# Performance work log

Hardware: AMD Instinct MI355X
Metric: run time of the kernel (lower is better)

## Reference

```python
import jax, jax.numpy as jnp
import numpy as np

N_NODES = 100000
N_EDGES = 400000
D_IN = 128
D_OUT = 128
BN_EPS = 1e-5


def setup_inputs() -> dict:
    key = jax.random.key(0)
    k1, k2, k3, k4, k5 = jax.random.split(key, 5)
    n_feat = jax.random.normal(k1, (N_NODES, D_IN), dtype=jnp.float32)
    edge_index = jax.random.randint(k2, (2, N_EDGES), 0, N_NODES, dtype=jnp.int32)
    edge_weight = jnp.ones((N_EDGES,), dtype=jnp.float32)
    # learned params: BatchNorm1d affine + Linear(in, out, bias=False)
    gamma = jnp.ones((D_IN,), dtype=jnp.float32) + 0.1 * jax.random.normal(k3, (D_IN,), dtype=jnp.float32)
    beta = 0.1 * jax.random.normal(k4, (D_IN,), dtype=jnp.float32)
    W = jax.random.normal(k5, (D_OUT, D_IN), dtype=jnp.float32) * (1.0 / np.sqrt(D_IN))
    return {"n_feat": n_feat, "edge_index": edge_index, "edge_weight": edge_weight,
            "gamma": gamma, "beta": beta, "W": W}


def reference(n_feat, edge_index, edge_weight, gamma, beta, W):
    # BatchNorm1d (training-mode batch stats, biased variance) -> ReLU -> Linear (no bias)
    mu = jnp.mean(n_feat, axis=0)
    var = jnp.mean(jnp.square(n_feat - mu), axis=0)
    xh = (n_feat - mu) * jax.lax.rsqrt(var + BN_EPS)
    y = jax.nn.relu(gamma * xh + beta)
    h = y @ W.T  # [N, D_OUT]
    # sparse adjacency matmul: out[row] += w * h[col]
    row, col = edge_index[0], edge_index[1]
    msgs = h[col] * edge_weight[:, None]          # gather, [E, D_OUT]
    agg = jax.ops.segment_sum(msgs, row, num_segments=N_NODES)
    return h * h + agg
```

## Files before the change

### kernel.cpp

```cpp
#include <hip/hip_runtime.h>

#define N_NODES 100000
#define N_EDGES 400000
#define D 128
#define BN_EPS 1e-5f
#define ELL_CAP 32

#define NSTAT 64
#define CS_BLOCKS 625
#define CS_ITER 20

#define WS_STATS   0
#define WS_HB      (NSTAT * 256)
#define WS_DEG2    (WS_HB + N_NODES * D / 2)
#define WS_ELL2    (WS_DEG2 + N_NODES)
#define WS_ELL2_END (WS_ELL2 + N_NODES * ELL_CAP * 2)
#define WS_WB      WS_ELL2_END
#define WS_SCL     (WS_WB + 8192)
#define WS_SHF     (WS_SCL + 128)
#define WS_ELL_END2 (WS_SHF + 128)
#define WS_SCALE   (NSTAT * 256)
#define WS_SHIFT   (WS_SCALE + 128)
#define WS_WT      (WS_SHIFT + 128)
#define WS_H       (WS_WT + D * D)
#define WS_DEG     (WS_H + N_NODES * D)
#define WS_ROWPTR  (WS_DEG + N_NODES)
#define WS_CURSOR  (WS_ROWPTR + N_NODES + 1)
#define WS_CSRCOL  (WS_CURSOR + N_NODES)
#define WS_CSRW    (WS_CSRCOL + N_EDGES)
#define WS_END     (WS_CSRW + N_EDGES)

typedef __attribute__((ext_vector_type(8))) short short8;
typedef __attribute__((ext_vector_type(4))) float f32x4;

static __device__ __forceinline__ unsigned short f2bf(float f) {
    union { float f; unsigned u; } v; v.f = f;
    unsigned r = v.u + 0x7FFF + ((v.u >> 16) & 1);
    return (unsigned short)(r >> 16);
}
static __device__ __forceinline__ float bf2f(unsigned short b) {
    union { unsigned u; float f; } v; v.u = ((unsigned)b) << 16;
    return v.f;
}
static __device__ __forceinline__ unsigned short f2h(float f) {
    union { _Float16 h; unsigned short u; } v; v.h = (_Float16)f;
    return v.u;
}
static __device__ __forceinline__ float h2f(unsigned short u) {
    union { unsigned short u; _Float16 h; } v; v.u = u;
    return (float)v.h;
}

__global__ __launch_bounds__(256) void colstats_kernel(const float* __restrict__ x,
                                                       float* __restrict__ stats,
                                                       int* __restrict__ deg) {
    int tid = blockIdx.x * 256 + threadIdx.x;
    if (deg && tid < N_NODES) deg[tid] = 0;
    const int NTH = CS_BLOCKS * 256;
    const float4* x4 = (const float4*)x;
    float4 v[CS_ITER];
    #pragma unroll
    for (int i = 0; i < CS_ITER; i++) v[i] = x4[tid + i * NTH];
    float4 s = {0.f, 0.f, 0.f, 0.f};
    float4 q = {0.f, 0.f, 0.f, 0.f};
    #pragma unroll
    for (int i = 0; i < CS_ITER; i++) {
        s.x += v[i].x; s.y += v[i].y; s.z += v[i].z; s.w += v[i].w;
        q.x += v[i].x * v[i].x; q.y += v[i].y * v[i].y;
        q.z += v[i].z * v[i].z; q.w += v[i].w * v[i].w;
    }

    __shared__ float4 ss[256];
    __shared__ float4 sq[256];
    ss[threadIdx.x] = s;
    sq[threadIdx.x] = q;
    __syncthreads();
    if (threadIdx.x < 32) {
        float4 a = ss[threadIdx.x];
        float4 b = sq[threadIdx.x];
        for (int i = 32; i < 256; i += 32) {
            float4 t1 = ss[threadIdx.x + i];
            float4 t2 = sq[threadIdx.x + i];
            a.x += t1.x; a.y += t1.y; a.z += t1.z; a.w += t1.w;
            b.x += t2.x; b.y += t2.y; b.z += t2.z; b.w += t2.w;
        }
        float* st = stats + (blockIdx.x % NSTAT) * 256;
        int colb = (threadIdx.x * 4) & 127;
        atomicAdd(&st[colb + 0], a.x);
        atomicAdd(&st[colb + 1], a.y);
        atomicAdd(&st[colb + 2], a.z);
        atomicAdd(&st[colb + 3], a.w);
        atomicAdd(&st[128 + colb + 0], b.x);
        atomicAdd(&st[128 + colb + 1], b.y);
        atomicAdd(&st[128 + colb + 2], b.z);
        atomicAdd(&st[128 + colb + 3], b.w);
    }
}

__global__ __launch_bounds__(256) void fill_ell2_kernel(const int* __restrict__ ei,
                                                        const float* __restrict__ ew,
                                                        int* __restrict__ deg,
                                                        int2* __restrict__ ell2) {
    int e = blockIdx.x * 256 + threadIdx.x;
    if (e >= N_EDGES) return;
    int r = ei[e];
    int c = ei[N_EDGES + e];
    float w = ew[e];
    int slot = atomicAdd(&deg[r], 1);
    if (slot < ELL_CAP) ell2[r * ELL_CAP + slot] = make_int2(c, __float_as_int(w));
}

__global__ __launch_bounds__(256) void convw_finalize_kernel(const float* __restrict__ W,
                                                             const float* __restrict__ stats,
                                                             const float* __restrict__ gamma,
                                                             const float* __restrict__ beta,
                                                             unsigned short* __restrict__ Wb,
                                                             float* __restrict__ scale,
                                                             float* __restrict__ shift) {
    int b = blockIdx.x;
    int t = threadIdx.x;
    if (b < 16) {
        int i = b * 256 + t;
        float4 v = *(const float4*)(W + i * 4);
        ushort4 o;
        o.x = f2bf(v.x); o.y = f2bf(v.y); o.z = f2bf(v.z); o.w = f2bf(v.w);
        *(ushort4*)(Wb + i * 4) = o;
    } else if (t < 128) {
        float sum = 0.f, sq = 0.f;
        #pragma unroll 16
        for (int c = 0; c < NSTAT; c++) {
            sum += stats[c * 256 + t];
            sq  += stats[c * 256 + 128 + t];
        }
        float mu  = sum * (1.0f / N_NODES);
        float var = sq * (1.0f / N_NODES) - mu * mu;
        float sc  = gamma[t] * rsqrtf(var + BN_EPS);
        scale[t] = sc;
        shift[t] = beta[t] - mu * sc;
    }
}

#define YPAD 136
__global__ __launch_bounds__(256, 2) void gemm_mfma4_kernel(const float* __restrict__ x,
                                                            const float* __restrict__ scale,
                                                            const float* __restrict__ shift,
                                                            const unsigned short* __restrict__ Wb,
                                                            unsigned short* __restrict__ hh) {
    __shared__ __align__(16) unsigned short Yl[64 * YPAD];
    int t = threadIdx.x;
    int row0 = blockIdx.x * 64;
    int lane = t & 63;
    int wave = t >> 6;
    int m16  = lane & 15;
    int quad = lane >> 4;
    int wrow0 = wave * 16;
    int c4 = (t & 31) * 4;

    float4 sc = *(const float4*)(scale + c4);
    float4 sh = *(const float4*)(shift + c4);
    float4 xv[8];
    #pragma unroll
    for (int p = 0; p < 8; p++) {
        int r = (t + p * 256) >> 5;
        int grow = row0 + r;
        int srow = grow < N_NODES ? grow : N_NODES - 1;
        xv[p] = *(const float4*)(x + (size_t)srow * D + c4);
    }
    const unsigned short* wb = Wb + m16 * D + quad * 8;
    short8 bfr[4][8];
    #pragma unroll
    for (int kc = 0; kc < 4; kc++) {
        #pragma unroll
        for (int nt = 0; nt < 8; nt++) {
            bfr[kc][nt] = *(const short8*)(wb + nt * 16 * D + kc * 32);
        }
    }
    #pragma unroll
    for (int p = 0; p < 8; p++) {
        int r = (t + p * 256) >> 5;
        ushort4 y;
        y.x = f2bf(fmaxf(fmaf(xv[p].x, sc.x, sh.x), 0.f));
        y.y = f2bf(fmaxf(fmaf(xv[p].y, sc.y, sh.y), 0.f));
        y.z = f2bf(fmaxf(fmaf(xv[p].z, sc.z, sh.z), 0.f));
        y.w = f2bf(fmaxf(fmaf(xv[p].w, sc.w, sh.w), 0.f));
        *(ushort4*)(Yl + r * YPAD + c4) = y;
    }
    __syncthreads();

    f32x4 acc[8];
    #pragma unroll
    for (int nt = 0; nt < 8; nt++) acc[nt] = (f32x4){0.f, 0.f, 0.f, 0.f};

    const unsigned short* yl = Yl + (wrow0 + m16) * YPAD + quad * 8;
    #pragma unroll
    for (int kc = 0; kc < 4; kc++) {
        short8 a = *(const short8*)(yl + kc * 32);
        #pragma unroll
        for (int nt = 0; nt < 8; nt++) {
            acc[nt] = __builtin_amdgcn_mfma_f32_16x16x32_bf16(a, bfr[kc][nt], acc[nt], 0, 0, 0);
        }
    }

    #pragma unroll
    for (int r = 0; r < 4; r++) {
        int grow = row0 + wrow0 + quad * 4 + r;
        if (grow < N_NODES) {
            unsigned short* hrow = hh + (size_t)grow * D + m16;
            #pragma unroll
            for (int nt = 0; nt < 8; nt++) {
                hrow[nt * 16] = f2h(acc[nt][r]);
            }
        }
    }
}

__global__ __launch_bounds__(256) void gather_ell3_kernel(const int* __restrict__ deg,
                                                          const int2* __restrict__ ell2,
                                                          const unsigned short* __restrict__ hh,
                                                          float* __restrict__ out) {
    int lane = threadIdx.x & 15;
    int n = blockIdx.x * 16 + (threadIdx.x >> 4);
    if (n >= N_NODES) return;
    short8 hself = *(const short8*)(hh + (size_t)n * D + lane * 8);
    int dg = deg[n];
    if (dg > ELL_CAP) dg = ELL_CAP;
    int dg16 = dg < 16 ? dg : 16;

    int2 my = make_int2(0, 0);
    if (lane < dg16) my = ell2[n * ELL_CAP + lane];

    float acc[8] = {0.f, 0.f, 0.f, 0.f, 0.f, 0.f, 0.f, 0.f};
    int s = 0;
    for (; s + 4 <= dg16; s += 4) {
        int   c0 = __shfl(my.x, s + 0, 16); float w0 = __int_as_float(__shfl(my.y, s + 0, 16));
        int   c1 = __shfl(my.x, s + 1, 16); float w1 = __int_as_float(__shfl(my.y, s + 1, 16));
        int   c2 = __shfl(my.x, s + 2, 16); float w2 = __int_as_float(__shfl(my.y, s + 2, 16));
        int   c3 = __shfl(my.x, s + 3, 16); float w3 = __int_as_float(__shfl(my.y, s + 3, 16));
        short8 v0 = *(const short8*)(hh + (size_t)c0 * D + lane * 8);
        short8 v1 = *(const short8*)(hh + (size_t)c1 * D + lane * 8);
        short8 v2 = *(const short8*)(hh + (size_t)c2 * D + lane * 8);
        short8 v3 = *(const short8*)(hh + (size_t)c3 * D + lane * 8);
        #pragma unroll
        for (int j = 0; j < 8; j++) {
            acc[j] = fmaf(w0, h2f((unsigned short)v0[j]), acc[j]);
            acc[j] = fmaf(w1, h2f((unsigned short)v1[j]), acc[j]);
            acc[j] = fmaf(w2, h2f((unsigned short)v2[j]), acc[j]);
            acc[j] = fmaf(w3, h2f((unsigned short)v3[j]), acc[j]);
        }
    }
    for (; s < dg16; s++) {
        int c = __shfl(my.x, s, 16);
        float w = __int_as_float(__shfl(my.y, s, 16));
        short8 v = *(const short8*)(hh + (size_t)c * D + lane * 8);
        #pragma unroll
        for (int j = 0; j < 8; j++) acc[j] = fmaf(w, h2f((unsigned short)v[j]), acc[j]);
    }
    for (s = 16; s < dg; s++) {
        int2 cw = ell2[n * ELL_CAP + s];
        float w = __int_as_float(cw.y);
        short8 v = *(const short8*)(hh + (size_t)cw.x * D + lane * 8);
        #pragma unroll
        for (int j = 0; j < 8; j++) acc[j] = fmaf(w, h2f((unsigned short)v[j]), acc[j]);
    }

    float4 a, b;
    {
        float h0 = h2f((unsigned short)hself[0]); float h1 = h2f((unsigned short)hself[1]);
        float h2 = h2f((unsigned short)hself[2]); float h3 = h2f((unsigned short)hself[3]);
        float h4 = h2f((unsigned short)hself[4]); float h5 = h2f((unsigned short)hself[5]);
        float h6 = h2f((unsigned short)hself[6]); float h7 = h2f((unsigned short)hself[7]);
        a.x = fmaf(h0, h0, acc[0]); a.y = fmaf(h1, h1, acc[1]);
        a.z = fmaf(h2, h2, acc[2]); a.w = fmaf(h3, h3, acc[3]);
        b.x = fmaf(h4, h4, acc[4]); b.y = fmaf(h5, h5, acc[5]);
        b.z = fmaf(h6, h6, acc[6]); b.w = fmaf(h7, h7, acc[7]);
    }
    float* o = out + (size_t)n * D + lane * 8;
    *(float4*)o = a;
    *(float4*)(o + 4) = b;
}

__global__ __launch_bounds__(128) void finalize_kernel(const float* __restrict__ stats,
                                                       const float* __restrict__ gamma,
                                                       const float* __restrict__ beta,
                                                       float* __restrict__ scale,
                                                       float* __restrict__ shift) {
    int d = threadIdx.x;
    float sum = 0.f, sq = 0.f;
    #pragma unroll 16
    for (int c = 0; c < NSTAT; c++) {
        sum += stats[c * 256 + d];
        sq  += stats[c * 256 + 128 + d];
    }
    float mu  = sum * (1.0f / N_NODES);
    float var = sq * (1.0f / N_NODES) - mu * mu;
    float sc  = gamma[d] * rsqrtf(var + BN_EPS);
    scale[d] = sc;
    shift[d] = beta[d] - mu * sc;
}

__global__ __launch_bounds__(256) void transposeW_kernel(const float* __restrict__ W,
                                                         float* __restrict__ Wt) {
    int i = blockIdx.x * blockDim.x + threadIdx.x;
    if (i < D * D) {
        int j = i >> 7;
        int k = i & 127;
        Wt[k * D + j] = W[i];
    }
}

template <int WRITE_SQ>
__global__ __launch_bounds__(256) void gemm_kernel(const float* __restrict__ x,
                                                   const float* __restrict__ scale,
                                                   const float* __restrict__ shift,
                                                   const float* __restrict__ Wt,
                                                   float* __restrict__ h,
                                                   float* __restrict__ out) {
    __shared__ float Ws[D * D];
    __shared__ float Ys[32 * D];
    int t = threadIdx.x;
    const float4* Wt4 = (const float4*)Wt;
    float4* Ws4 = (float4*)Ws;
    #pragma unroll 4
    for (int i = t; i < D * D / 4; i += 256) Ws4[i] = Wt4[i];
    int row0 = blockIdx.x * 32;
    const float4* x4 = (const float4*)(x + (size_t)row0 * D);
    float4* Ys4 = (float4*)Ys;
    #pragma unroll 2
    for (int i = t; i < 32 * D / 4; i += 256) {
        int c4 = (i & 31) * 4;
        float4 v = x4[i];
        v.x = fmaxf(fmaf(v.x, scale[c4 + 0], shift[c4 + 0]), 0.f);
        v.y = fmaxf(fmaf(v.y, scale[c4 + 1], shift[c4 + 1]), 0.f);
        v.z = fmaxf(fmaf(v.z, scale[c4 + 2], shift[c4 + 2]), 0.f);
        v.w = fmaxf(fmaf(v.w, scale[c4 + 3], shift[c4 + 3]), 0.f);
        Ys4[i] = v;
    }
    __syncthreads();
    int cg = t & 31;
    int rg = t >> 5;
    float4 acc[4] = {{0,0,0,0},{0,0,0,0},{0,0,0,0},{0,0,0,0}};
    #pragma unroll 2
    for (int k = 0; k < D; k += 4) {
        float4 w0 = *(const float4*)&Ws[(k + 0) * D + cg * 4];
        float4 w1 = *(const float4*)&Ws[(k + 1) * D + cg * 4];
        float4 w2 = *(const float4*)&Ws[(k + 2) * D + cg * 4];
        float4 w3 = *(const float4*)&Ws[(k + 3) * D + cg * 4];
        #pragma unroll
        for (int r = 0; r < 4; r++) {
            float4 y = *(const float4*)&Ys[(rg * 4 + r) * D + k];
            acc[r].x = fmaf(y.x, w0.x, fmaf(y.y, w1.x, fmaf(y.z, w2.x, fmaf(y.w, w3.x, acc[r].x))));
            acc[r].y = fmaf(y.x, w0.y, fmaf(y.y, w1.y, fmaf(y.z, w2.y, fmaf(y.w, w3.y, acc[r].y))));
            acc[r].z = fmaf(y.x, w0.z, fmaf(y.y, w1.z, fmaf(y.z, w2.z, fmaf(y.w, w3.z, acc[r].z))));
            acc[r].w = fmaf(y.x, w0.w, fmaf(y.y, w1.w, fmaf(y.z, w2.w, fmaf(y.w, w3.w, acc[r].w))));
        }
    }
    #pragma unroll
    for (int r = 0; r < 4; r++) {
        size_t row = (size_t)row0 + rg * 4 + r;
        float4 v = acc[r];
        *(float4*)&h[row * D + cg * 4] = v;
        if (WRITE_SQ) {
            float4 sqv = {v.x * v.x, v.y * v.y, v.z * v.z, v.w * v.w};
            *(float4*)&out[row * D + cg * 4] = sqv;
        }
    }
}

__global__ __launch_bounds__(256) void hist_kernel(const int* __restrict__ ei,
                                                   int* __restrict__ deg) {
    int e = blockIdx.x * 256 + threadIdx.x;
    if (e < N_EDGES) atomicAdd(&deg[ei[e]], 1);
}

__global__ __launch_bounds__(1024) void scan_kernel(const int* __restrict__ deg,
                                                    int* __restrict__ row_ptr,
                                                    int* __restrict__ cursor) {
    __shared__ int part[1024];
    int t = threadIdx.x;
    const int CHUNK = 100;
    int base = t * CHUNK;
    int s = 0;
    if (base < N_NODES) {
        for (int i = 0; i < CHUNK; i++) s += deg[base + i];
    }
    part[t] = s;
    __syncthreads();
    for (int off = 1; off < 1024; off <<= 1) {
        int v = (t >= off) ? part[t - off] : 0;
        __syncthreads();
        part[t] += v;
        __syncthreads();
    }
    int pre = (t == 0) ? 0 : part[t - 1];
    if (base < N_NODES) {
        for (int i = 0; i < CHUNK; i++) {
            row_ptr[base + i] = pre;
            cursor[base + i] = pre;
            pre += deg[base + i];
        }
    }
    if (t == 1023) row_ptr[N_NODES] = part[1023];
}

__global__ __launch_bounds__(256) void fill_kernel(const int* __restrict__ ei,
                                                   const float* __restrict__ ew,
                                                   int* __restrict__ cursor,
                                                   int* __restrict__ csr_col,
                                                   float* __restrict__ csr_w) {
    int e = blockIdx.x * 256 + threadIdx.x;
    if (e >= N_EDGES) return;
    int r = ei[e];
    int c = ei[N_EDGES + e];
    int slot = atomicAdd(&cursor[r], 1);
    csr_col[slot] = c;
    csr_w[slot] = ew[e];
}

__global__ __launch_bounds__(256) void gather_kernel(const int* __restrict__ row_ptr,
                                                     const int* __restrict__ csr_col,
                                                     const float* __restrict__ csr_w,
                                                     const float* __restrict__ h,
                                                     float* __restrict__ out) {
    int lane = threadIdx.x & 31;
    int n = blockIdx.x * 8 + (threadIdx.x >> 5);
    if (n >= N_NODES) return;
    int s0 = row_ptr[n];
    int s1 = row_ptr[n + 1];
    float4 acc = {0.f, 0.f, 0.f, 0.f};
    for (int s = s0; s < s1; s++) {
        int c = csr_col[s];
        float w = csr_w[s];
        float4 v = *(const float4*)&h[(size_t)c * D + lane * 4];
        acc.x = fmaf(w, v.x, acc.x);
        acc.y = fmaf(w, v.y, acc.y);
        acc.z = fmaf(w, v.z, acc.z);
        acc.w = fmaf(w, v.w, acc.w);
    }
    float4 hv = *(const float4*)&h[(size_t)n * D + lane * 4];
    float4 o;
    o.x = fmaf(hv.x, hv.x, acc.x);
    o.y = fmaf(hv.y, hv.y, acc.y);
    o.z = fmaf(hv.z, hv.z, acc.z);
    o.w = fmaf(hv.w, hv.w, acc.w);
    *(float4*)&out[(size_t)n * D + lane * 4] = o;
}

__global__ __launch_bounds__(256) void scatter_kernel(const int* __restrict__ ei,
                                                      const float* __restrict__ ew,
                                                      const float* __restrict__ h,
                                                      float* __restrict__ out) {
    int lane = threadIdx.x & 31;
    int e = blockIdx.x * 8 + (threadIdx.x >> 5);
    if (e >= N_EDGES) return;
    int r = ei[e];
    int c = ei[N_EDGES + e];
    float w = ew[e];
    float4 v = *(const float4*)&h[(size_t)c * D + lane * 4];
    float* o = out + (size_t)r * D + lane * 4;
    atomicAdd(o + 0, v.x * w);
    atomicAdd(o + 1, v.y * w);
    atomicAdd(o + 2, v.z * w);
    atomicAdd(o + 3, v.w * w);
}

extern "C" void kernel_launch(void* const* d_in, const int* in_sizes, int n_in,
                              void* d_out, int out_size, void* d_ws, size_t ws_size,
                              hipStream_t stream) {
    const float* n_feat = (const float*)d_in[0];
    const int*   ei     = (const int*)d_in[1];
    const float* ew     = (const float*)d_in[2];
    const float* gamma  = (const float*)d_in[3];
    const float* beta   = (const float*)d_in[4];
    const float* W      = (const float*)d_in[5];
    float* out = (float*)d_out;

    float* ws    = (float*)d_ws;
    float* stats = ws + WS_STATS;

    bool ell_ok = ws_size >= (size_t)WS_ELL_END2 * sizeof(float);
    bool csr_ok = ws_size >= (size_t)WS_END * sizeof(float);

    hipMemsetAsync(stats, 0, NSTAT * 256 * sizeof(float), stream);

    if (ell_ok) {
        unsigned short* hh  = (unsigned short*)(ws + WS_HB);
        int*  deg  = (int*)ws + WS_DEG2;
        int2* ell2 = (int2*)((int*)ws + WS_ELL2);
        unsigned short* Wb = (unsigned short*)(ws + WS_WB);
        float* scl = ws + WS_SCL;
        float* shf = ws + WS_SHF;

        colstats_kernel<<<CS_BLOCKS, 256, 0, stream>>>(n_feat, stats, deg);
        fill_ell2_kernel<<<(N_EDGES + 255) / 256, 256, 0, stream>>>(ei, ew, deg, ell2);
        convw_finalize_kernel<<<17, 256, 0, stream>>>(W, stats, gamma, beta, Wb, scl, shf);
        gemm_mfma4_kernel<<<(N_NODES + 63) / 64, 256, 0, stream>>>(n_feat, scl, shf, Wb, hh);
        gather_ell3_kernel<<<(N_NODES + 15) / 16, 256, 0, stream>>>(deg, ell2, hh, out);
    } else if (csr_ok) {
        float* scale = ws + WS_SCALE;
        float* shift = ws + WS_SHIFT;
        float* Wt    = ws + WS_WT;
        float* h     = ws + WS_H;
        int*   deg     = (int*)ws + WS_DEG;
        int*   row_ptr = (int*)ws + WS_ROWPTR;
        int*   cursor  = (int*)ws + WS_CURSOR;
        int*   csr_col = (int*)ws + WS_CSRCOL;
        float* csr_w   = ws + WS_CSRW;

        colstats_kernel<<<CS_BLOCKS, 256, 0, stream>>>(n_feat, stats, nullptr);
        finalize_kernel<<<1, 128, 0, stream>>>(stats, gamma, beta, scale, shift);
        transposeW_kernel<<<64, 256, 0, stream>>>(W, Wt);
        hipMemsetAsync(deg, 0, N_NODES * sizeof(int), stream);
        gemm_kernel<0><<<N_NODES / 32, 256, 0, stream>>>(n_feat, scale, shift, Wt, h, out);
        hist_kernel<<<(N_EDGES + 255) / 256, 256, 0, stream>>>(ei, deg);
        scan_kernel<<<1, 1024, 0, stream>>>(deg, row_ptr, cursor);
        fill_kernel<<<(N_EDGES + 255) / 256, 256, 0, stream>>>(ei, ew, cursor, csr_col, csr_w);
        gather_kernel<<<(N_NODES + 7) / 8, 256, 0, stream>>>(row_ptr, csr_col, csr_w, h, out);
    } else {
        float* scale = ws + WS_SCALE;
        float* shift = ws + WS_SHIFT;
        float* Wt    = ws + WS_WT;
        float* h     = ws + WS_H;
        colstats_kernel<<<CS_BLOCKS, 256, 0, stream>>>(n_feat, stats, nullptr);
        finalize_kernel<<<1, 128, 0, stream>>>(stats, gamma, beta, scale, shift);
        transposeW_kernel<<<64, 256, 0, stream>>>(W, Wt);
        gemm_kernel<1><<<N_NODES / 32, 256, 0, stream>>>(n_feat, scale, shift, Wt, h, out);
        scatter_kernel<<<(N_EDGES + 7) / 8, 256, 0, stream>>>(ei, ew, h, out);
    }
}
```

Before: 195.1 us.

## Fuse ELL fill with weight conversion, raise GEMM occupancy, batch gather per lane group

Merges the edge-to-ELL fill kernel with the weight-conversion/BN-finalize kernel into one launch, removing a launch gap. The GEMM kernel no longer preloads all B fragments into registers and instead loads them inside the MFMA loop, with launch bounds raised to 4 blocks per SM for higher occupancy. The gather kernel now has each 16-lane group process 4 nodes in an interleaved loop, so more independent loads are in flight. This trades register-held weights for repeated global/L1 loads and adds per-node divergence checks in the gather. It also reads ELL entries beyond each node's degree, which are likely uninitialized but only shuffled when used.

```diff
diff --git a/kernel.cpp b/kernel.cpp
--- a/kernel.cpp
+++ b/kernel.cpp
@@ -9,6 +9,7 @@
 #define NSTAT 64
 #define CS_BLOCKS 625
 #define CS_ITER 20
+#define FILL_BLOCKS 1563
 
 #define WS_STATS   0
 #define WS_HB      (NSTAT * 256)
@@ -97,30 +98,29 @@
     }
 }
 
-__global__ __launch_bounds__(256) void fill_ell2_kernel(const int* __restrict__ ei,
-                                                        const float* __restrict__ ew,
-                                                        int* __restrict__ deg,
-                                                        int2* __restrict__ ell2) {
-    int e = blockIdx.x * 256 + threadIdx.x;
-    if (e >= N_EDGES) return;
-    int r = ei[e];
-    int c = ei[N_EDGES + e];
-    float w = ew[e];
-    int slot = atomicAdd(&deg[r], 1);
-    if (slot < ELL_CAP) ell2[r * ELL_CAP + slot] = make_int2(c, __float_as_int(w));
-}
-
-__global__ __launch_bounds__(256) void convw_finalize_kernel(const float* __restrict__ W,
-                                                             const float* __restrict__ stats,
-                                                             const float* __restrict__ gamma,
-                                                             const float* __restrict__ beta,
-                                                             unsigned short* __restrict__ Wb,
-                                                             float* __restrict__ scale,
-                                                             float* __restrict__ shift) {
+__global__ __launch_bounds__(256) void fill_ell2_convw_kernel(const int* __restrict__ ei,
+                                                              const float* __restrict__ ew,
+                                                              int* __restrict__ deg,
+                                                              int2* __restrict__ ell2,
+                                                              const float* __restrict__ W,
+                                                              const float* __restrict__ stats,
+                                                              const float* __restrict__ gamma,
+                                                              const float* __restrict__ beta,
+                                                              unsigned short* __restrict__ Wb,
+                                                              float* __restrict__ scale,
+                                                              float* __restrict__ shift) {
     int b = blockIdx.x;
     int t = threadIdx.x;
-    if (b < 16) {
-        int i = b * 256 + t;
+    if (b < FILL_BLOCKS) {
+        int e = b * 256 + t;
+        if (e >= N_EDGES) return;
+        int r = ei[e];
+        int c = ei[N_EDGES + e];
+        float w = ew[e];
+        int slot = atomicAdd(&deg[r], 1);
+        if (slot < ELL_CAP) ell2[r * ELL_CAP + slot] = make_int2(c, __float_as_int(w));
+    } else if (b < FILL_BLOCKS + 16) {
+        int i = (b - FILL_BLOCKS) * 256 + t;
         float4 v = *(const float4*)(W + i * 4);
         ushort4 o;
         o.x = f2bf(v.x); o.y = f2bf(v.y); o.z = f2bf(v.z); o.w = f2bf(v.w);
@@ -141,7 +141,7 @@
 }
 
 #define YPAD 136
-__global__ __launch_bounds__(256, 2) void gemm_mfma4_kernel(const float* __restrict__ x,
+__global__ __launch_bounds__(256, 4) void gemm_mfma5_kernel(const float* __restrict__ x,
                                                             const float* __restrict__ scale,
                                                             const float* __restrict__ shift,
                                                             const unsigned short* __restrict__ Wb,
@@ -166,15 +166,6 @@
         int srow = grow < N_NODES ? grow : N_NODES - 1;
         xv[p] = *(const float4*)(x + (size_t)srow * D + c4);
     }
-    const unsigned short* wb = Wb + m16 * D + quad * 8;
-    short8 bfr[4][8];
-    #pragma unroll
-    for (int kc = 0; kc < 4; kc++) {
-        #pragma unroll
-        for (int nt = 0; nt < 8; nt++) {
-            bfr[kc][nt] = *(const short8*)(wb + nt * 16 * D + kc * 32);
-        }
-    }
     #pragma unroll
     for (int p = 0; p < 8; p++) {
         int r = (t + p * 256) >> 5;
@@ -191,13 +182,15 @@
     #pragma unroll
     for (int nt = 0; nt < 8; nt++) acc[nt] = (f32x4){0.f, 0.f, 0.f, 0.f};
 
+    const unsigned short* wb = Wb + m16 * D + quad * 8;
     const unsigned short* yl = Yl + (wrow0 + m16) * YPAD + quad * 8;
     #pragma unroll
     for (int kc = 0; kc < 4; kc++) {
         short8 a = *(const short8*)(yl + kc * 32);
         #pragma unroll
         for (int nt = 0; nt < 8; nt++) {
-            acc[nt] = __builtin_amdgcn_mfma_f32_16x16x32_bf16(a, bfr[kc][nt], acc[nt], 0, 0, 0);
+            short8 b = *(const short8*)(wb + nt * 16 * D + kc * 32);
+            acc[nt] = __builtin_amdgcn_mfma_f32_16x16x32_bf16(a, b, acc[nt], 0, 0, 0);
         }
     }
 
@@ -214,69 +207,79 @@
     }
 }
 
-__global__ __launch_bounds__(256) void gather_ell3_kernel(const int* __restrict__ deg,
+__global__ __launch_bounds__(256) void gather_ell4_kernel(const int* __restrict__ deg,
                                                           const int2* __restrict__ ell2,
                                                           const unsigned short* __restrict__ hh,
                                                           float* __restrict__ out) {
     int lane = threadIdx.x & 15;
-    int n = blockIdx.x * 16 + (threadIdx.x >> 4);
-    if (n >= N_NODES) return;
-    short8 hself = *(const short8*)(hh + (size_t)n * D + lane * 8);
-    int dg = deg[n];
-    if (dg > ELL_CAP) dg = ELL_CAP;
-    int dg16 = dg < 16 ? dg : 16;
-
-    int2 my = make_int2(0, 0);
-    if (lane < dg16) my = ell2[n * ELL_CAP + lane];
-
-    float acc[8] = {0.f, 0.f, 0.f, 0.f, 0.f, 0.f, 0.f, 0.f};
-    int s = 0;
-    for (; s + 4 <= dg16; s += 4) {
-        int   c0 = __shfl(my.x, s + 0, 16); float w0 = __int_as_float(__shfl(my.y, s + 0, 16));
-        int   c1 = __shfl(my.x, s + 1, 16); float w1 = __int_as_float(__shfl(my.y, s + 1, 16));
-        int   c2 = __shfl(my.x, s + 2, 16); float w2 = __int_as_float(__shfl(my.y, s + 2, 16));
-        int   c3 = __shfl(my.x, s + 3, 16); float w3 = __int_as_float(__shfl(my.y, s + 3, 16));
-        short8 v0 = *(const short8*)(hh + (size_t)c0 * D + lane * 8);
-        short8 v1 = *(const short8*)(hh + (size_t)c1 * D + lane * 8);
-        short8 v2 = *(const short8*)(hh + (size_t)c2 * D + lane * 8);
-        short8 v3 = *(const short8*)(hh + (size_t)c3 * D + lane * 8);
+    int g = blockIdx.x * 16 + (threadIdx.x >> 4);
+    int n0 = g * 4;
+    if (n0 >= N_NODES) return;
+
+    int dgf[4], dg16[4];
+    #pragma unroll
+    for (int j = 0; j < 4; j++) {
+        int d = deg[n0 + j];
+        dgf[j] = d > ELL_CAP ? ELL_CAP : d;
+        dg16[j] = dgf[j] < 16 ? dgf[j] : 16;
+    }
+    int2 my[4];
+    #pragma unroll
+    for (int j = 0; j < 4; j++) my[j] = ell2[(size_t)(n0 + j) * ELL_CAP + lane];
+    short8 hself[4];
+    #pragma unroll
+    for (int j = 0; j < 4; j++) hself[j] = *(const short8*)(hh + (size_t)(n0 + j) * D + lane * 8);
+
+    float acc[4][8];
+    #pragma unroll
+    for (int j = 0; j < 4; j++)
         #pragma unroll
-        for (int j = 0; j < 8; j++) {
-            acc[j] = fmaf(w0, h2f((unsigned short)v0[j]), acc[j]);
-            acc[j] = fmaf(w1, h2f((unsigned short)v1[j]), acc[j]);
-            acc[j] = fmaf(w2, h2f((unsigned short)v2[j]), acc[j]);
-            acc[j] = fmaf(w3, h2f((unsigned short)v3[j]), acc[j]);
-        }
-    }
-    for (; s < dg16; s++) {
-        int c = __shfl(my.x, s, 16);
-        float w = __int_as_float(__shfl(my.y, s, 16));
-        short8 v = *(const short8*)(hh + (size_t)c * D + lane * 8);
+        for (int k = 0; k < 8; k++) acc[j][k] = 0.f;
+
+    int dmax = dg16[0];
+    dmax = dg16[1] > dmax ? dg16[1] : dmax;
+    dmax = dg16[2] > dmax ? dg16[2] : dmax;
+    dmax = dg16[3] > dmax ? dg16[3] : dmax;
+
+    #pragma unroll 2
+    for (int s = 0; s < dmax; s++) {
         #pragma unroll
-        for (int j = 0; j < 8; j++) acc[j] = fmaf(w, h2f((unsigned short)v[j]), acc[j]);
-    }
-    for (s = 16; s < dg; s++) {
-        int2 cw = ell2[n * ELL_CAP + s];
-        float w = __int_as_float(cw.y);
-        short8 v = *(const short8*)(hh + (size_t)cw.x * D + lane * 8);
-        #pragma unroll
-        for (int j = 0; j < 8; j++) acc[j] = fmaf(w, h2f((unsigned short)v[j]), acc[j]);
-    }
-
-    float4 a, b;
-    {
-        float h0 = h2f((unsigned short)hself[0]); float h1 = h2f((unsigned short)hself[1]);
-        float h2 = h2f((unsigned short)hself[2]); float h3 = h2f((unsigned short)hself[3]);
-        float h4 = h2f((unsigned short)hself[4]); float h5 = h2f((unsigned short)hself[5]);
-        float h6 = h2f((unsigned short)hself[6]); float h7 = h2f((unsigned short)hself[7]);
-        a.x = fmaf(h0, h0, acc[0]); a.y = fmaf(h1, h1, acc[1]);
-        a.z = fmaf(h2, h2, acc[2]); a.w = fmaf(h3, h3, acc[3]);
-        b.x = fmaf(h4, h4, acc[4]); b.y = fmaf(h5, h5, acc[5]);
-        b.z = fmaf(h6, h6, acc[6]); b.w = fmaf(h7, h7, acc[7]);
-    }
-    float* o = out + (size_t)n * D + lane * 8;
-    *(float4*)o = a;
-    *(float4*)(o + 4) = b;
+        for (int j = 0; j < 4; j++) {
+            if (s < dg16[j]) {
+                int   c = __shfl(my[j].x, s, 16);
+                float w = __int_as_float(__shfl(my[j].y, s, 16));
+                short8 v = *(const short8*)(hh + (size_t)c * D + lane * 8);
+                #pragma unroll
+                for (int k = 0; k < 8; k++) acc[j][k] = fmaf(w, h2f((unsigned short)v[k]), acc[j][k]);
+            }
+        }
+    }
+    #pragma unroll
+    for (int j = 0; j < 4; j++) {
+        for (int s = 16; s < dgf[j]; s++) {
+            int2 cw = ell2[(size_t)(n0 + j) * ELL_CAP + s];
+            float w = __int_as_float(cw.y);
+            short8 v = *(const short8*)(hh + (size_t)cw.x * D + lane * 8);
+            #pragma unroll
+            for (int k = 0; k < 8; k++) acc[j][k] = fmaf(w, h2f((unsigned short)v[k]), acc[j][k]);
+        }
+    }
+
+    #pragma unroll
+    for (int j = 0; j < 4; j++) {
+        float4 a, b;
+        float h0 = h2f((unsigned short)hself[j][0]); float h1 = h2f((unsigned short)hself[j][1]);
+        float h2 = h2f((unsigned short)hself[j][2]); float h3 = h2f((unsigned short)hself[j][3]);
+        float h4 = h2f((unsigned short)hself[j][4]); float h5 = h2f((unsigned short)hself[j][5]);
+        float h6 = h2f((unsigned short)hself[j][6]); float h7 = h2f((unsigned short)hself[j][7]);
+        a.x = fmaf(h0, h0, acc[j][0]); a.y = fmaf(h1, h1, acc[j][1]);
+        a.z = fmaf(h2, h2, acc[j][2]); a.w = fmaf(h3, h3, acc[j][3]);
+        b.x = fmaf(h4, h4, acc[j][4]); b.y = fmaf(h5, h5, acc[j][5]);
+        b.z = fmaf(h6, h6, acc[j][6]); b.w = fmaf(h7, h7, acc[j][7]);
+        float* o = out + (size_t)(n0 + j) * D + lane * 8;
+        *(float4*)o = a;
+        *(float4*)(o + 4) = b;
+    }
 }
 
 __global__ __launch_bounds__(128) void finalize_kernel(const float* __restrict__ stats,
@@ -491,10 +494,10 @@
         float* shf = ws + WS_SHF;
 
         colstats_kernel<<<CS_BLOCKS, 256, 0, stream>>>(n_feat, stats, deg);
-        fill_ell2_kernel<<<(N_EDGES + 255) / 256, 256, 0, stream>>>(ei, ew, deg, ell2);
-        convw_finalize_kernel<<<17, 256, 0, stream>>>(W, stats, gamma, beta, Wb, scl, shf);
-        gemm_mfma4_kernel<<<(N_NODES + 63) / 64, 256, 0, stream>>>(n_feat, scl, shf, Wb, hh);
-        gather_ell3_kernel<<<(N_NODES + 15) / 16, 256, 0, stream>>>(deg, ell2, hh, out);
+        fill_ell2_convw_kernel<<<FILL_BLOCKS + 17, 256, 0, stream>>>(ei, ew, deg, ell2,
+                                                                     W, stats, gamma, beta, Wb, scl, shf);
+        gemm_mfma5_kernel<<<(N_NODES + 63) / 64, 256, 0, stream>>>(n_feat, scl, shf, Wb, hh);
+        gather_ell4_kernel<<<(N_NODES / 4 + 15) / 16, 256, 0, stream>>>(deg, ell2, hh, out);
     } else if (csr_ok) {
         float* scale = ws + WS_SCALE;
         float* shift = ws + WS_SHIFT;
```

Measured after the change: 197.5 us. No clear change (+1.2%).

## Fuse colstats, ELL fill and W conversion into one kernel; fold BN finalize into GEMM

Applied to the files above, without the earlier changes.

The separate column-stats, ELL fill and W-to-bf16 kernels are merged into one launch that splits work by block index, and the deg zeroing moves to a memset. The BN scale/shift computation is now done in every GEMM block, which removes the finalize launch. The GEMM no longer preloads W fragments into registers and uses a launch bound of 4 blocks instead of 2 to raise occupancy. The gather uses nontemporal loads and stores. Together these cut launch count and serialization, at the cost of redundant stats reduction per GEMM block and more W reloads.

```diff
diff --git a/kernel.cpp b/kernel.cpp
--- a/kernel.cpp
+++ b/kernel.cpp
@@ -9,6 +9,7 @@
 #define NSTAT 64
 #define CS_BLOCKS 625
 #define CS_ITER 20
+#define FILL_BLOCKS 1563
 
 #define WS_STATS   0
 #define WS_HB      (NSTAT * 256)
@@ -16,9 +17,7 @@
 #define WS_ELL2    (WS_DEG2 + N_NODES)
 #define WS_ELL2_END (WS_ELL2 + N_NODES * ELL_CAP * 2)
 #define WS_WB      WS_ELL2_END
-#define WS_SCL     (WS_WB + 8192)
-#define WS_SHF     (WS_SCL + 128)
-#define WS_ELL_END2 (WS_SHF + 128)
+#define WS_ELL_END2 (WS_WB + 8192)
 #define WS_SCALE   (NSTAT * 256)
 #define WS_SHIFT   (WS_SCALE + 128)
 #define WS_WT      (WS_SHIFT + 128)
@@ -51,6 +50,223 @@
     return (float)v.h;
 }
 
+__global__ __launch_bounds__(256) void fused_pre_kernel(const float* __restrict__ x,
+                                                        float* __restrict__ stats,
+                                                        const int* __restrict__ ei,
+                                                        const float* __restrict__ ew,
+                                                        int* __restrict__ deg,
+                                                        int2* __restrict__ ell2,
+                                                        const float* __restrict__ W,
+                                                        unsigned short* __restrict__ Wb) {
+    int b = blockIdx.x;
+    int t = threadIdx.x;
+    if (b < CS_BLOCKS) {
+        int tid = b * 256 + t;
+        const int NTH = CS_BLOCKS * 256;
+        const float4* x4 = (const float4*)x;
+        float4 v[CS_ITER];
+        #pragma unroll
+        for (int i = 0; i < CS_ITER; i++) v[i] = x4[tid + i * NTH];
+        float4 s = {0.f, 0.f, 0.f, 0.f};
+        float4 q = {0.f, 0.f, 0.f, 0.f};
+        #pragma unroll
+        for (int i = 0; i < CS_ITER; i++) {
+            s.x += v[i].x; s.y += v[i].y; s.z += v[i].z; s.w += v[i].w;
+            q.x += v[i].x * v[i].x; q.y += v[i].y * v[i].y;
+            q.z += v[i].z * v[i].z; q.w += v[i].w * v[i].w;
+        }
+        __shared__ float4 ss[256];
+        __shared__ float4 sq[256];
+        ss[t] = s;
+        sq[t] = q;
+        __syncthreads();
+        if (t < 32) {
+            float4 a = ss[t];
+            float4 bb = sq[t];
+            for (int i = 32; i < 256; i += 32) {
+                float4 t1 = ss[t + i];
+                float4 t2 = sq[t + i];
+                a.x += t1.x; a.y += t1.y; a.z += t1.z; a.w += t1.w;
+                bb.x += t2.x; bb.y += t2.y; bb.z += t2.z; bb.w += t2.w;
+            }
+            float* st = stats + (b % NSTAT) * 256;
+            int colb = (t * 4) & 127;
+            atomicAdd(&st[colb + 0], a.x);
+            atomicAdd(&st[colb + 1], a.y);
+            atomicAdd(&st[colb + 2], a.z);
+            atomicAdd(&st[colb + 3], a.w);
+            atomicAdd(&st[128 + colb + 0], bb.x);
+            atomicAdd(&st[128 + colb + 1], bb.y);
+            atomicAdd(&st[128 + colb + 2], bb.z);
+            atomicAdd(&st[128 + colb + 3], bb.w);
+        }
+    } else if (b < CS_BLOCKS + FILL_BLOCKS) {
+        int e = (b - CS_BLOCKS) * 256 + t;
+        if (e >= N_EDGES) return;
+        int r = ei[e];
+        int c = ei[N_EDGES + e];
+        float w = ew[e];
+        int slot = atomicAdd(&deg[r], 1);
+        if (slot < ELL_CAP) ell2[r * ELL_CAP + slot] = make_int2(c, __float_as_int(w));
+    } else {
+        int i = (b - CS_BLOCKS - FILL_BLOCKS) * 256 + t;
+        float4 v = *(const float4*)(W + i * 4);
+        ushort4 o;
+        o.x = f2bf(v.x); o.y = f2bf(v.y); o.z = f2bf(v.z); o.w = f2bf(v.w);
+        *(ushort4*)(Wb + i * 4) = o;
+    }
+}
+
+#define YPAD 136
+__global__ __launch_bounds__(256, 4) void gemm_mfma6_kernel(const float* __restrict__ x,
+                                                            const float* __restrict__ stats,
+                                                            const float* __restrict__ gamma,
+                                                            const float* __restrict__ beta,
+                                                            const unsigned short* __restrict__ Wb,
+                                                            unsigned short* __restrict__ hh) {
+    __shared__ __align__(16) unsigned short Yl[64 * YPAD];
+    __shared__ float sscale[128];
+    __shared__ float sshift[128];
+    int t = threadIdx.x;
+    int row0 = blockIdx.x * 64;
+    int lane = t & 63;
+    int wave = t >> 6;
+    int m16  = lane & 15;
+    int quad = lane >> 4;
+    int wrow0 = wave * 16;
+    int c4 = (t & 31) * 4;
+
+    float4 xv[8];
+    #pragma unroll
+    for (int p = 0; p < 8; p++) {
+        int r = (t + p * 256) >> 5;
+        int grow = row0 + r;
+        int srow = grow < N_NODES ? grow : N_NODES - 1;
+        xv[p] = *(const float4*)(x + (size_t)srow * D + c4);
+    }
+    if (t < 128) {
+        float sum = 0.f, sq = 0.f;
+        #pragma unroll 16
+        for (int c = 0; c < NSTAT; c++) {
+            sum += stats[c * 256 + t];
+            sq  += stats[c * 256 + 128 + t];
+        }
+        float mu  = sum * (1.0f / N_NODES);
+        float var = sq * (1.0f / N_NODES) - mu * mu;
+        float sc  = gamma[t] * rsqrtf(var + BN_EPS);
+        sscale[t] = sc;
+        sshift[t] = beta[t] - mu * sc;
+    }
+    __syncthreads();
+
+    float4 sc = *(const float4*)(sscale + c4);
+    float4 sh = *(const float4*)(sshift + c4);
+    #pragma unroll
+    for (int p = 0; p < 8; p++) {
+        int r = (t + p * 256) >> 5;
+        ushort4 y;
+        y.x = f2bf(fmaxf(fmaf(xv[p].x, sc.x, sh.x), 0.f));
+        y.y = f2bf(fmaxf(fmaf(xv[p].y, sc.y, sh.y), 0.f));
+        y.z = f2bf(fmaxf(fmaf(xv[p].z, sc.z, sh.z), 0.f));
+        y.w = f2bf(fmaxf(fmaf(xv[p].w, sc.w, sh.w), 0.f));
+        *(ushort4*)(Yl + r * YPAD + c4) = y;
+    }
+    __syncthreads();
+
+    f32x4 acc[8];
+    #pragma unroll
+    for (int nt = 0; nt < 8; nt++) acc[nt] = (f32x4){0.f, 0.f, 0.f, 0.f};
+
+    const unsigned short* wb = Wb + m16 * D + quad * 8;
+    const unsigned short* yl = Yl + (wrow0 + m16) * YPAD + quad * 8;
+    #pragma unroll
+    for (int kc = 0; kc < 4; kc++) {
+        short8 a = *(const short8*)(yl + kc * 32);
+        #pragma unroll
+        for (int nt = 0; nt < 8; nt++) {
+            short8 b = *(const short8*)(wb + nt * 16 * D + kc * 32);
+            acc[nt] = __builtin_amdgcn_mfma_f32_16x16x32_bf16(a, b, acc[nt], 0, 0, 0);
+        }
+    }
+
+    #pragma unroll
+    for (int r = 0; r < 4; r++) {
+        int grow = row0 + wrow0 + quad * 4 + r;
+        if (grow < N_NODES) {
+            unsigned short* hrow = hh + (size_t)grow * D + m16;
+            #pragma unroll
+            for (int nt = 0; nt < 8; nt++) {
+                hrow[nt * 16] = f2h(acc[nt][r]);
+            }
+        }
+    }
+}
+
+__global__ __launch_bounds__(256) void gather_ell6_kernel(const int* __restrict__ deg,
+                                                          const int2* __restrict__ ell2,
+                                                          const unsigned short* __restrict__ hh,
+                                                          float* __restrict__ out) {
+    int lane = threadIdx.x & 15;
+    int n = blockIdx.x * 16 + (threadIdx.x >> 4);
+    if (n >= N_NODES) return;
+    short8 hself = *(const short8*)(hh + (size_t)n * D + lane * 8);
+    int dg = __builtin_nontemporal_load(&deg[n]);
+    if (dg > ELL_CAP) dg = ELL_CAP;
+    int dg16 = dg < 16 ? dg : 16;
+
+    int2 my = make_int2(0, 0);
+    if (lane < dg16) my = ell2[n * ELL_CAP + lane];
+
+    float acc[8] = {0.f, 0.f, 0.f, 0.f, 0.f, 0.f, 0.f, 0.f};
+    int s = 0;
+    for (; s + 4 <= dg16; s += 4) {
+        int   c0 = __shfl(my.x, s + 0, 16); float w0 = __int_as_float(__shfl(my.y, s + 0, 16));
+        int   c1 = __shfl(my.x, s + 1, 16); float w1 = __int_as_float(__shfl(my.y, s + 1, 16));
+        int   c2 = __shfl(my.x, s + 2, 16); float w2 = __int_as_float(__shfl(my.y, s + 2, 16));
+        int   c3 = __shfl(my.x, s + 3, 16); float w3 = __int_as_float(__shfl(my.y, s + 3, 16));
+        short8 v0 = *(const short8*)(hh + (size_t)c0 * D + lane * 8);
+        short8 v1 = *(const short8*)(hh + (size_t)c1 * D + lane * 8);
+        short8 v2 = *(const short8*)(hh + (size_t)c2 * D + lane * 8);
+        short8 v3 = *(const short8*)(hh + (size_t)c3 * D + lane * 8);
+        #pragma unroll
+        for (int j = 0; j < 8; j++) {
+            acc[j] = fmaf(w0, h2f((unsigned short)v0[j]), acc[j]);
+            acc[j] = fmaf(w1, h2f((unsigned short)v1[j]), acc[j]);
+            acc[j] = fmaf(w2, h2f((unsigned short)v2[j]), acc[j]);
+            acc[j] = fmaf(w3, h2f((unsigned short)v3[j]), acc[j]);
+        }
+    }
+    for (; s < dg16; s++) {
+        int c = __shfl(my.x, s, 16);
+        float w = __int_as_float(__shfl(my.y, s, 16));
+        short8 v = *(const short8*)(hh + (size_t)c * D + lane * 8);
+        #pragma unroll
+        for (int j = 0; j < 8; j++) acc[j] = fmaf(w, h2f((unsigned short)v[j]), acc[j]);
+    }
+    for (s = 16; s < dg; s++) {
+        int2 cw = ell2[n * ELL_CAP + s];
+        float w = __int_as_float(cw.y);
+        short8 v = *(const short8*)(hh + (size_t)cw.x * D + lane * 8);
+        #pragma unroll
+        for (int j = 0; j < 8; j++) acc[j] = fmaf(w, h2f((unsigned short)v[j]), acc[j]);
+    }
+
+    f32x4 a, b;
+    {
+        float h0 = h2f((unsigned short)hself[0]); float h1 = h2f((unsigned short)hself[1]);
+        float h2 = h2f((unsigned short)hself[2]); float h3 = h2f((unsigned short)hself[3]);
+        float h4 = h2f((unsigned short)hself[4]); float h5 = h2f((unsigned short)hself[5]);
+        float h6 = h2f((unsigned short)hself[6]); float h7 = h2f((unsigned short)hself[7]);
+        a[0] = fmaf(h0, h0, acc[0]); a[1] = fmaf(h1, h1, acc[1]);
+        a[2] = fmaf(h2, h2, acc[2]); a[3] = fmaf(h3, h3, acc[3]);
+        b[0] = fmaf(h4, h4, acc[4]); b[1] = fmaf(h5, h5, acc[5]);
+        b[2] = fmaf(h6, h6, acc[6]); b[3] = fmaf(h7, h7, acc[7]);
+    }
+    float* o = out + (size_t)n * D + lane * 8;
+    __builtin_nontemporal_store(a, (f32x4*)o);
+    __builtin_nontemporal_store(b, (f32x4*)(o + 4));
+}
+
 __global__ __launch_bounds__(256) void colstats_kernel(const float* __restrict__ x,
                                                        float* __restrict__ stats,
                                                        int* __restrict__ deg) {
@@ -69,7 +285,6 @@
         q.x += v[i].x * v[i].x; q.y += v[i].y * v[i].y;
         q.z += v[i].z * v[i].z; q.w += v[i].w * v[i].w;
     }
-
     __shared__ float4 ss[256];
     __shared__ float4 sq[256];
     ss[threadIdx.x] = s;
@@ -95,188 +310,6 @@
         atomicAdd(&st[128 + colb + 2], b.z);
         atomicAdd(&st[128 + colb + 3], b.w);
     }
-}
-
-__global__ __launch_bounds__(256) void fill_ell2_kernel(const int* __restrict__ ei,
-                                                        const float* __restrict__ ew,
-                                                        int* __restrict__ deg,
-                                                        int2* __restrict__ ell2) {
-    int e = blockIdx.x * 256 + threadIdx.x;
-    if (e >= N_EDGES) return;
-    int r = ei[e];
-    int c = ei[N_EDGES + e];
-    float w = ew[e];
-    int slot = atomicAdd(&deg[r], 1);
-    if (slot < ELL_CAP) ell2[r * ELL_CAP + slot] = make_int2(c, __float_as_int(w));
-}
-
-__global__ __launch_bounds__(256) void convw_finalize_kernel(const float* __restrict__ W,
-                                                             const float* __restrict__ stats,
-                                                             const float* __restrict__ gamma,
-                                                             const float* __restrict__ beta,
-                                                             unsigned short* __restrict__ Wb,
-                                                             float* __restrict__ scale,
-                                                             float* __restrict__ shift) {
-    int b = blockIdx.x;
-    int t = threadIdx.x;
-    if (b < 16) {
-        int i = b * 256 + t;
-        float4 v = *(const float4*)(W + i * 4);
-        ushort4 o;
-        o.x = f2bf(v.x); o.y = f2bf(v.y); o.z = f2bf(v.z); o.w = f2bf(v.w);
-        *(ushort4*)(Wb + i * 4) = o;
-    } else if (t < 128) {
-        float sum = 0.f, sq = 0.f;
-        #pragma unroll 16
-        for (int c = 0; c < NSTAT; c++) {
-            sum += stats[c * 256 + t];
-            sq  += stats[c * 256 + 128 + t];
-        }
-        float mu  = sum * (1.0f / N_NODES);
-        float var = sq * (1.0f / N_NODES) - mu * mu;
-        float sc  = gamma[t] * rsqrtf(var + BN_EPS);
-        scale[t] = sc;
-        shift[t] = beta[t] - mu * sc;
-    }
-}
-
-#define YPAD 136
-__global__ __launch_bounds__(256, 2) void gemm_mfma4_kernel(const float* __restrict__ x,
-                                                            const float* __restrict__ scale,
-                                                            const float* __restrict__ shift,
-                                                            const unsigned short* __restrict__ Wb,
-                                                            unsigned short* __restrict__ hh) {
-    __shared__ __align__(16) unsigned short Yl[64 * YPAD];
-    int t = threadIdx.x;
-    int row0 = blockIdx.x * 64;
-    int lane = t & 63;
-    int wave = t >> 6;
-    int m16  = lane & 15;
-    int quad = lane >> 4;
-    int wrow0 = wave * 16;
-    int c4 = (t & 31) * 4;
-
-    float4 sc = *(const float4*)(scale + c4);
-    float4 sh = *(const float4*)(shift + c4);
-    float4 xv[8];
-    #pragma unroll
-    for (int p = 0; p < 8; p++) {
-        int r = (t + p * 256) >> 5;
-        int grow = row0 + r;
-        int srow = grow < N_NODES ? grow : N_NODES - 1;
-        xv[p] = *(const float4*)(x + (size_t)srow * D + c4);
-    }
-    const unsigned short* wb = Wb + m16 * D + quad * 8;
-    short8 bfr[4][8];
-    #pragma unroll
-    for (int kc = 0; kc < 4; kc++) {
-        #pragma unroll
-        for (int nt = 0; nt < 8; nt++) {
-            bfr[kc][nt] = *(const short8*)(wb + nt * 16 * D + kc * 32);
-        }
-    }
-    #pragma unroll
-    for (int p = 0; p < 8; p++) {
-        int r = (t + p * 256) >> 5;
-        ushort4 y;
-        y.x = f2bf(fmaxf(fmaf(xv[p].x, sc.x, sh.x), 0.f));
-        y.y = f2bf(fmaxf(fmaf(xv[p].y, sc.y, sh.y), 0.f));
-        y.z = f2bf(fmaxf(fmaf(xv[p].z, sc.z, sh.z), 0.f));
-        y.w = f2bf(fmaxf(fmaf(xv[p].w, sc.w, sh.w), 0.f));
-        *(ushort4*)(Yl + r * YPAD + c4) = y;
-    }
-    __syncthreads();
-
-    f32x4 acc[8];
-    #pragma unroll
-    for (int nt = 0; nt < 8; nt++) acc[nt] = (f32x4){0.f, 0.f, 0.f, 0.f};
-
-    const unsigned short* yl = Yl + (wrow0 + m16) * YPAD + quad * 8;
-    #pragma unroll
-    for (int kc = 0; kc < 4; kc++) {
-        short8 a = *(const short8*)(yl + kc * 32);
-        #pragma unroll
-        for (int nt = 0; nt < 8; nt++) {
-            acc[nt] = __builtin_amdgcn_mfma_f32_16x16x32_bf16(a, bfr[kc][nt], acc[nt], 0, 0, 0);
-        }
-    }
-
-    #pragma unroll
-    for (int r = 0; r < 4; r++) {
-        int grow = row0 + wrow0 + quad * 4 + r;
-        if (grow < N_NODES) {
-            unsigned short* hrow = hh + (size_t)grow * D + m16;
-            #pragma unroll
-            for (int nt = 0; nt < 8; nt++) {
-                hrow[nt * 16] = f2h(acc[nt][r]);
-            }
-        }
-    }
-}
-
-__global__ __launch_bounds__(256) void gather_ell3_kernel(const int* __restrict__ deg,
-                                                          const int2* __restrict__ ell2,
-                                                          const unsigned short* __restrict__ hh,
-                                                          float* __restrict__ out) {
-    int lane = threadIdx.x & 15;
-    int n = blockIdx.x * 16 + (threadIdx.x >> 4);
-    if (n >= N_NODES) return;
-    short8 hself = *(const short8*)(hh + (size_t)n * D + lane * 8);
-    int dg = deg[n];
-    if (dg > ELL_CAP) dg = ELL_CAP;
-    int dg16 = dg < 16 ? dg : 16;
-
-    int2 my = make_int2(0, 0);
-    if (lane < dg16) my = ell2[n * ELL_CAP + lane];
-
-    float acc[8] = {0.f, 0.f, 0.f, 0.f, 0.f, 0.f, 0.f, 0.f};
-    int s = 0;
-    for (; s + 4 <= dg16; s += 4) {
-        int   c0 = __shfl(my.x, s + 0, 16); float w0 = __int_as_float(__shfl(my.y, s + 0, 16));
-        int   c1 = __shfl(my.x, s + 1, 16); float w1 = __int_as_float(__shfl(my.y, s + 1, 16));
-        int   c2 = __shfl(my.x, s + 2, 16); float w2 = __int_as_float(__shfl(my.y, s + 2, 16));
-        int   c3 = __shfl(my.x, s + 3, 16); float w3 = __int_as_float(__shfl(my.y, s + 3, 16));
-        short8 v0 = *(const short8*)(hh + (size_t)c0 * D + lane * 8);
-        short8 v1 = *(const short8*)(hh + (size_t)c1 * D + lane * 8);
-        short8 v2 = *(const short8*)(hh + (size_t)c2 * D + lane * 8);
-        short8 v3 = *(const short8*)(hh + (size_t)c3 * D + lane * 8);
-        #pragma unroll
-        for (int j = 0; j < 8; j++) {
-            acc[j] = fmaf(w0, h2f((unsigned short)v0[j]), acc[j]);
-            acc[j] = fmaf(w1, h2f((unsigned short)v1[j]), acc[j]);
-            acc[j] = fmaf(w2, h2f((unsigned short)v2[j]), acc[j]);
-            acc[j] = fmaf(w3, h2f((unsigned short)v3[j]), acc[j]);
-        }
-    }
-    for (; s < dg16; s++) {
-        int c = __shfl(my.x, s, 16);
-        float w = __int_as_float(__shfl(my.y, s, 16));
-        short8 v = *(const short8*)(hh + (size_t)c * D + lane * 8);
-        #pragma unroll
-        for (int j = 0; j < 8; j++) acc[j] = fmaf(w, h2f((unsigned short)v[j]), acc[j]);
-    }
-    for (s = 16; s < dg; s++) {
-        int2 cw = ell2[n * ELL_CAP + s];
-        float w = __int_as_float(cw.y);
-        short8 v = *(const short8*)(hh + (size_t)cw.x * D + lane * 8);
-        #pragma unroll
-        for (int j = 0; j < 8; j++) acc[j] = fmaf(w, h2f((unsigned short)v[j]), acc[j]);
-    }
-
-    float4 a, b;
-    {
-        float h0 = h2f((unsigned short)hself[0]); float h1 = h2f((unsigned short)hself[1]);
-        float h2 = h2f((unsigned short)hself[2]); float h3 = h2f((unsigned short)hself[3]);
-        float h4 = h2f((unsigned short)hself[4]); float h5 = h2f((unsigned short)hself[5]);
-        float h6 = h2f((unsigned short)hself[6]); float h7 = h2f((unsigned short)hself[7]);
-        a.x = fmaf(h0, h0, acc[0]); a.y = fmaf(h1, h1, acc[1]);
-        a.z = fmaf(h2, h2, acc[2]); a.w = fmaf(h3, h3, acc[3]);
-        b.x = fmaf(h4, h4, acc[4]); b.y = fmaf(h5, h5, acc[5]);
-        b.z = fmaf(h6, h6, acc[6]); b.w = fmaf(h7, h7, acc[7]);
-    }
-    float* o = out + (size_t)n * D + lane * 8;
-    *(float4*)o = a;
-    *(float4*)(o + 4) = b;
 }
 
 __global__ __launch_bounds__(128) void finalize_kernel(const float* __restrict__ stats,
@@ -480,21 +513,19 @@
     bool ell_ok = ws_size >= (size_t)WS_ELL_END2 * sizeof(float);
     bool csr_ok = ws_size >= (size_t)WS_END * sizeof(float);
 
-    hipMemsetAsync(stats, 0, NSTAT * 256 * sizeof(float), stream);
+    (void)hipMemsetAsync(stats, 0, NSTAT * 256 * sizeof(float), stream);
 
     if (ell_ok) {
         unsigned short* hh  = (unsigned short*)(ws + WS_HB);
         int*  deg  = (int*)ws + WS_DEG2;
         int2* ell2 = (int2*)((int*)ws + WS_ELL2);
         unsigned short* Wb = (unsigned short*)(ws + WS_WB);
-        float* scl = ws + WS_SCL;
-        float* shf = ws + WS_SHF;
-
-        colstats_kernel<<<CS_BLOCKS, 256, 0, stream>>>(n_feat, stats, deg);
-        fill_ell2_kernel<<<(N_EDGES + 255) / 256, 256, 0, stream>>>(ei, ew, deg, ell2);
-        convw_finalize_kernel<<<17, 256, 0, stream>>>(W, stats, gamma, beta, Wb, scl, shf);
-        gemm_mfma4_kernel<<<(N_NODES + 63) / 64, 256, 0, stream>>>(n_feat, scl, shf, Wb, hh);
-        gather_ell3_kernel<<<(N_NODES + 15) / 16, 256, 0, stream>>>(deg, ell2, hh, out);
+
+        (void)hipMemsetAsync(deg, 0, N_NODES * sizeof(int), stream);
+        fused_pre_kernel<<<CS_BLOCKS + FILL_BLOCKS + 16, 256, 0, stream>>>(
+            n_feat, stats, ei, ew, deg, ell2, W, Wb);
+        gemm_mfma6_kernel<<<(N_NODES + 63) / 64, 256, 0, stream>>>(n_feat, stats, gamma, beta, Wb, hh);
+        gather_ell6_kernel<<<(N_NODES + 15) / 16, 256, 0, stream>>>(deg, ell2, hh, out);
     } else if (csr_ok) {
         float* scale = ws + WS_SCALE;
         float* shift = ws + WS_SHIFT;
@@ -509,7 +540,7 @@
         colstats_kernel<<<CS_BLOCKS, 256, 0, stream>>>(n_feat, stats, nullptr);
         finalize_kernel<<<1, 128, 0, stream>>>(stats, gamma, beta, scale, shift);
         transposeW_kernel<<<64, 256, 0, stream>>>(W, Wt);
-        hipMemsetAsync(deg, 0, N_NODES * sizeof(int), stream);
+        (void)hipMemsetAsync(deg, 0, N_NODES * sizeof(int), stream);
         gemm_kernel<0><<<N_NODES / 32, 256, 0, stream>>>(n_feat, scale, shift, Wt, h, out);
         hist_kernel<<<(N_EDGES + 255) / 256, 256, 0, stream>>>(ei, deg);
         scan_kernel<<<1, 1024, 0, stream>>>(deg, row_ptr, cursor);
```

New measurement: 195.9 us. Within noise of the previous version (+0.4%).
